# Kernel tuning notes

Hardware: AMD Instinct MI355X
Metric: run time of the kernel (lower is better)

## Reference

```python
import jax, jax.numpy as jnp
import numpy as np

D = 256
H = 8
DK = D // H
FF = 4 * D
EPS = 1e-5


def layer_norm(x, g, b):
    mu = jnp.mean(x, axis=-1, keepdims=True)
    var = jnp.mean(jnp.square(x - mu), axis=-1, keepdims=True)
    return (x - mu) * jax.lax.rsqrt(var + EPS) * g + b


def setup_inputs() -> dict:
    key = jax.random.key(0)
    ks = jax.random.split(key, 12)
    s = 0.02
    return {
        "x": jax.random.normal(ks[0], (4, 2048, D), jnp.float32),
        "Wq": jax.random.normal(ks[1], (D, D), jnp.float32) * s,
        "Wk": jax.random.normal(ks[2], (D, D), jnp.float32) * s,
        "Wv": jax.random.normal(ks[3], (D, D), jnp.float32) * s,
        "Wo": jax.random.normal(ks[4], (D, D), jnp.float32) * s,
        "W1": jax.random.normal(ks[5], (D, FF), jnp.float32) * s,
        "W2": jax.random.normal(ks[6], (D, FF), jnp.float32) * s,
        "Wout": jax.random.normal(ks[7], (FF, D), jnp.float32) * s,
        "g1": jnp.ones((D,), jnp.float32),
        "b1": jnp.zeros((D,), jnp.float32),
        "g2": jnp.ones((D,), jnp.float32),
        "b2": jnp.zeros((D,), jnp.float32),
    }


def reference(x, Wq, Wk, Wv, Wo, W1, W2, Wout, g1, b1, g2, b2):
    B, S, _ = x.shape
    # --- multi-head attention (manual matmul + softmax + matmul) ---
    q = (x @ Wq).reshape(B, S, H, DK).transpose(0, 2, 1, 3)  # [B,H,S,DK]
    k = (x @ Wk).reshape(B, S, H, DK).transpose(0, 2, 1, 3)
    v = (x @ Wv).reshape(B, S, H, DK).transpose(0, 2, 1, 3)
    scores = jnp.einsum("bhqd,bhkd->bhqk", q, k) * (DK ** -0.5)  # [B,H,S,S]
    probs = jax.nn.softmax(scores, axis=-1)
    o = jnp.einsum("bhqk,bhkd->bhqd", probs, v)
    attn = o.transpose(0, 2, 1, 3).reshape(B, S, D) @ Wo
    # --- GLU feedforward with dual LayerNorms ---
    x1 = layer_norm(x + attn, g1, b1)
    xw = jax.nn.silu(x1 @ W1)
    xv = x1 @ W2
    out = (xw * xv) @ Wout
    return layer_norm(x1 + out, g2, b2)
```

## Files before the change

kernel.cpp:

```cpp
#include <hip/hip_runtime.h>

#define D 256
#define H 8
#define DK 32
#define FF 1024
#define SEQ 2048
#define BATCH 4
#define MROWS (BATCH * SEQ)
#define LN_EPS 1e-5f
#define QSCALE (0.1767766952966369f * 1.4426950408889634f)
#define LOG2E 1.4426950408889634f

typedef unsigned short u16;
typedef unsigned int u32;
typedef __attribute__((ext_vector_type(8))) short bf16x8;
typedef __attribute__((ext_vector_type(4))) float f32x4;

#define MFMA16(a, b, c) __builtin_amdgcn_mfma_f32_16x16x32_bf16(a, b, c, 0, 0, 0)

#if __has_builtin(__builtin_amdgcn_exp2f)
#define EXP2(x) __builtin_amdgcn_exp2f(x)
#else
#define EXP2(x) exp2f(x)
#endif
#if __has_builtin(__builtin_amdgcn_rcpf)
#define RCPF(x) __builtin_amdgcn_rcpf(x)
#else
#define RCPF(x) (1.f / (x))
#endif

__device__ __forceinline__ u16 f2bf(float f) {
    union { float f; u32 u; } x; x.f = f;
    u32 r = x.u + 0x7fffu + ((x.u >> 16) & 1u);
    return (u16)(r >> 16);
}
__device__ __forceinline__ u32 pack2(float a, float b) {
    return (u32)f2bf(a) | ((u32)f2bf(b) << 16);
}
__device__ __forceinline__ u32 pktrunc(float a, float b) {
    u32 ua = __builtin_bit_cast(u32, a), ub = __builtin_bit_cast(u32, b);
    return __builtin_amdgcn_perm(ub, ua, 0x07060302u);
}
__device__ __forceinline__ float silu_f(float x) {
    return x * RCPF(1.f + EXP2(-x * LOG2E));
}

__global__ void stage_w(const float* __restrict__ Wq, const float* __restrict__ Wk,
                        const float* __restrict__ Wv, const float* __restrict__ Wo,
                        const float* __restrict__ W1, const float* __restrict__ W2,
                        const float* __restrict__ Wout, u16* __restrict__ dst) {
    __shared__ float T[64][65];
    int bid = blockIdx.x, tid = threadIdx.x;
    const float* src;
    size_t dbase;
    int K, N, tile;
    float sc = 1.f;
    if (bid < 64) {
        int which = bid >> 4;
        tile = bid & 15;
        src = which == 0 ? Wq : which == 1 ? Wk : which == 2 ? Wv : Wo;
        if (which == 0) sc = QSCALE;
        dbase = (size_t)which << 16;
        K = 256; N = 256;
    } else if (bid < 192) {
        int which = (bid - 64) >> 6;
        tile = (bid - 64) & 63;
        src = which ? W2 : W1;
        dbase = 262144 + (size_t)which * 262144;
        K = 256; N = 1024;
    } else {
        tile = bid - 192;
        src = Wout;
        dbase = 786432;
        K = 1024; N = 256;
    }
    int ntn = N >> 6;
    int k0 = (tile / ntn) << 6, n0 = (tile % ntn) << 6;
#pragma unroll
    for (int p = 0; p < 4; p++) {
        int r = p * 16 + (tid >> 4), c = (tid & 15) * 4;
        float4 v = *(const float4*)(src + (size_t)(k0 + r) * N + n0 + c);
        T[c + 0][r] = v.x * sc;
        T[c + 1][r] = v.y * sc;
        T[c + 2][r] = v.z * sc;
        T[c + 3][r] = v.w * sc;
    }
    __syncthreads();
#pragma unroll
    for (int p = 0; p < 4; p++) {
        int n = p * 16 + (tid >> 4), k = (tid & 15) * 4;
        uint2 o;
        o.x = pack2(T[n][k], T[n][k + 1]);
        o.y = pack2(T[n][k + 2], T[n][k + 3]);
        *(uint2*)(dst + dbase + (size_t)(n0 + n) * K + k0 + k) = o;
    }
}

__global__ void gemm_qkv(const float* __restrict__ X, const u16* __restrict__ Bt,
                         u16* __restrict__ Qo, u16* __restrict__ Ko,
                         u16* __restrict__ Vo) {
    int gid = (blockIdx.x * 256 + threadIdx.x) >> 6;
    int lane = threadIdx.x & 63;
    int mt = gid / 12, ng = gid - mt * 12;
    int m0 = mt << 5, n0 = ng << 6;
    int m = lane & 15, quad = lane >> 4;
    const float* xp0 = X + (size_t)(m0 + m) * D + quad * 8;
    const float* xp1 = xp0 + (size_t)16 * D;
    const u16* bp = Bt + (size_t)(n0 + m) * D + quad * 8;
    f32x4 acc[2][4] = {{{0,0,0,0},{0,0,0,0},{0,0,0,0},{0,0,0,0}},
                       {{0,0,0,0},{0,0,0,0},{0,0,0,0},{0,0,0,0}}};
    for (int k0 = 0; k0 < D; k0 += 32) {
        float4 f0 = *(const float4*)(xp0 + k0);
        float4 f1 = *(const float4*)(xp0 + k0 + 4);
        float4 f2 = *(const float4*)(xp1 + k0);
        float4 f3 = *(const float4*)(xp1 + k0 + 4);
        uint4 u0, u1;
        u0.x = pktrunc(f0.x, f0.y); u0.y = pktrunc(f0.z, f0.w);
        u0.z = pktrunc(f1.x, f1.y); u0.w = pktrunc(f1.z, f1.w);
        u1.x = pktrunc(f2.x, f2.y); u1.y = pktrunc(f2.z, f2.w);
        u1.z = pktrunc(f3.x, f3.y); u1.w = pktrunc(f3.z, f3.w);
        bf16x8 a0 = __builtin_bit_cast(bf16x8, u0);
        bf16x8 a1 = __builtin_bit_cast(bf16x8, u1);
#pragma unroll
        for (int t = 0; t < 4; t++) {
            bf16x8 bv = *(const bf16x8*)(bp + (size_t)t * 16 * D + k0);
            acc[0][t] = MFMA16(a0, bv, acc[0][t]);
            acc[1][t] = MFMA16(a1, bv, acc[1][t]);
        }
    }
    int seg = n0 >> 8;
    int nc0 = n0 & 255;
    if (seg < 2) {
        u16* out = seg ? Ko : Qo;
#pragma unroll
        for (int u = 0; u < 2; u++) {
            int row = m0 + u * 16 + (quad << 2);
#pragma unroll
            for (int t = 0; t < 4; t++) {
                int col = nc0 + t * 16 + m;
#pragma unroll
                for (int r = 0; r < 4; r++)
                    out[(size_t)(row + r) * D + col] = f2bf(acc[u][t][r]);
            }
        }
    } else {
#pragma unroll
        for (int u = 0; u < 2; u++) {
            int row = m0 + u * 16 + (quad << 2);
            int b = row >> 11, sl = row & 2047;
#pragma unroll
            for (int t = 0; t < 4; t++) {
                int col = nc0 + t * 16 + m;
                int hh = col >> 5, dk = col & 31;
                size_t base = ((size_t)(b * 8 + hh) * 32 + dk) * SEQ + sl;
                uint2 pk;
                pk.x = pack2(acc[u][t][0], acc[u][t][1]);
                pk.y = pack2(acc[u][t][2], acc[u][t][3]);
                *(uint2*)(Vo + base) = pk;
            }
        }
    }
}

__global__ __launch_bounds__(256, 8)
void attn_mfma(const u16* __restrict__ Q, const u16* __restrict__ Km,
               const u16* __restrict__ Vt, u16* __restrict__ O) {
    __shared__ __align__(16) u16 Kt[2][64][36];
    __shared__ __align__(16) u16 Vl[2][32][68];
    int tid = threadIdx.x;
    int lane = tid & 63;
    int m = lane & 15, quad = lane >> 4;
    int w = tid >> 6;
    int bid = blockIdx.x;
    int qb = bid & 63;
    int bh = bid >> 6;
    int b = bh >> 3, h = bh & 7;
    int q0 = qb * 32 + (w & 1) * 16;
    int hb = w >> 1;
    size_t rowbase = (size_t)b * SEQ;

    bf16x8 qa = *(const bf16x8*)(Q + (rowbase + q0 + m) * D + h * DK + quad * 8);

    const u16* kg = Km + rowbase * D + h * DK;
    const u16* vg = Vt + (size_t)bh * DK * SEQ;

    int krow = tid >> 2, kseg = tid & 3;
    int skv = (krow & 32) | (((krow >> 2) & 3) << 3) | (((krow >> 4) & 1) << 2) | (krow & 3);
    int vrow = tid >> 3, vseg = tid & 7;

    uint4 kreg = *(const uint4*)(kg + (size_t)skv * D + kseg * 8);
    uint4 vreg = *(const uint4*)(vg + (size_t)vrow * SEQ + vseg * 8);
    *(uint4*)(&Kt[0][krow][kseg * 8]) = kreg;
    *(uint4*)(&Vl[0][vrow][vseg * 8]) = vreg;

    f32x4 o0 = {0,0,0,0}, o1 = {0,0,0,0};
    float ls = 0.f;

    for (int i = 0; i < SEQ / 64; i++) {
        int buf = i & 1;
        if (i + 1 < SEQ / 64) {
            int kvn = (i + 1) * 64;
            kreg = *(const uint4*)(kg + (size_t)(kvn + skv) * D + kseg * 8);
            vreg = *(const uint4*)(vg + (size_t)vrow * SEQ + kvn + vseg * 8);
        }
        __syncthreads();
        f32x4 z = {0,0,0,0};
        f32x4 s0, s1;
        {
            bf16x8 kb0 = *(const bf16x8*)(&Kt[buf][(2 * hb) * 16 + m][quad * 8]);
            bf16x8 kb1 = *(const bf16x8*)(&Kt[buf][(2 * hb + 1) * 16 + m][quad * 8]);
            s0 = MFMA16(kb0, qa, z);
            s1 = MFMA16(kb1, qa, z);
        }
        {
            float pa0 = EXP2(s0[0]), pa1 = EXP2(s0[1]);
            float pa2 = EXP2(s0[2]), pa3 = EXP2(s0[3]);
            float pb0 = EXP2(s1[0]), pb1 = EXP2(s1[1]);
            float pb2 = EXP2(s1[2]), pb3 = EXP2(s1[3]);
            ls += ((pa0 + pa1) + (pa2 + pa3)) + ((pb0 + pb1) + (pb2 + pb3));
            uint4 pw;
            pw.x = pktrunc(pa0, pa1);
            pw.y = pktrunc(pa2, pa3);
            pw.z = pktrunc(pb0, pb1);
            pw.w = pktrunc(pb2, pb3);
            bf16x8 pfrag = __builtin_bit_cast(bf16x8, pw);
            bf16x8 vb0 = *(const bf16x8*)(&Vl[buf][m][hb * 32 + quad * 8]);
            bf16x8 vb1 = *(const bf16x8*)(&Vl[buf][16 + m][hb * 32 + quad * 8]);
            o0 = MFMA16(pfrag, vb0, o0);
            o1 = MFMA16(pfrag, vb1, o1);
        }
        if (i + 1 < SEQ / 64) {
            *(uint4*)(&Kt[buf ^ 1][krow][kseg * 8]) = kreg;
            *(uint4*)(&Vl[buf ^ 1][vrow][vseg * 8]) = vreg;
        }
    }
    ls += __shfl_xor(ls, 16);
    ls += __shfl_xor(ls, 32);
    __syncthreads();
    float* comb = (float*)&Kt[0][0][0];
    if (w >= 2) {
        float* c = comb + ((size_t)(w - 2) * 64 + lane) * 9;
#pragma unroll
        for (int r = 0; r < 4; r++) { c[r] = o0[r]; c[4 + r] = o1[r]; }
        c[8] = ls;
    }
    __syncthreads();
    if (w < 2) {
        const float* c = comb + ((size_t)w * 64 + lane) * 9;
#pragma unroll
        for (int r = 0; r < 4; r++) { o0[r] += c[r]; o1[r] += c[4 + r]; }
        ls += c[8];
        u16* ob = O + (rowbase + q0 + quad * 4) * D + h * DK;
#pragma unroll
        for (int r = 0; r < 4; r++) {
            float lr = __shfl(ls, quad * 4 + r);
            float inv = 1.f / lr;
            ob[(size_t)r * D + m] = f2bf(o0[r] * inv);
            ob[(size_t)r * D + 16 + m] = f2bf(o1[r] * inv);
        }
    }
}

__global__ __launch_bounds__(256, 2)
void wo_res_ln(const u16* __restrict__ A, const u16* __restrict__ Bt,
               const float* __restrict__ res, const float* __restrict__ g,
               const float* __restrict__ bb, float* __restrict__ outf) {
    __shared__ float Sy[4][16], Sq[4][16], Mu[16], Rs[16];
    int tid = threadIdx.x;
    int w = tid >> 6, lane = tid & 63;
    int m = lane & 15, quad = lane >> 4;
    int m0 = blockIdx.x << 4, n0 = w << 6;
    const u16* ap = A + (size_t)(m0 + m) * D + quad * 8;
    const u16* bp = Bt + (size_t)(n0 + m) * D + quad * 8;
    f32x4 acc[4] = {{0,0,0,0},{0,0,0,0},{0,0,0,0},{0,0,0,0}};
#pragma unroll
    for (int k0 = 0; k0 < D; k0 += 32) {
        bf16x8 a0 = *(const bf16x8*)(ap + k0);
#pragma unroll
        for (int t = 0; t < 4; t++)
            acc[t] = MFMA16(a0, *(const bf16x8*)(bp + (size_t)t * 16 * D + k0), acc[t]);
    }
#pragma unroll
    for (int r = 0; r < 4; r++) {
        int row = (quad << 2) + r;
        float sy = 0.f, sq = 0.f;
#pragma unroll
        for (int t = 0; t < 4; t++) {
            float y = acc[t][r] + res[(size_t)(m0 + row) * D + n0 + t * 16 + m];
            acc[t][r] = y;
            sy += y;
            sq += y * y;
        }
        sy += __shfl_xor(sy, 1); sq += __shfl_xor(sq, 1);
        sy += __shfl_xor(sy, 2); sq += __shfl_xor(sq, 2);
        sy += __shfl_xor(sy, 4); sq += __shfl_xor(sq, 4);
        sy += __shfl_xor(sy, 8); sq += __shfl_xor(sq, 8);
        if (m == 0) { Sy[w][row] = sy; Sq[w][row] = sq; }
    }
    __syncthreads();
    if (tid < 16) {
        float s = Sy[0][tid] + Sy[1][tid] + Sy[2][tid] + Sy[3][tid];
        float q = Sq[0][tid] + Sq[1][tid] + Sq[2][tid] + Sq[3][tid];
        float mu = s * (1.f / 256.f);
        float var = q * (1.f / 256.f) - mu * mu;
        Mu[tid] = mu;
        Rs[tid] = rsqrtf(var + LN_EPS);
    }
    __syncthreads();
#pragma unroll
    for (int r = 0; r < 4; r++) {
        int row = (quad << 2) + r;
        float mu = Mu[row], rs = Rs[row];
#pragma unroll
        for (int t = 0; t < 4; t++) {
            int col = n0 + t * 16 + m;
            outf[(size_t)(m0 + row) * D + col] = (acc[t][r] - mu) * rs * g[col] + bb[col];
        }
    }
}

__global__ __launch_bounds__(1024, 4)
void ff_fused(const float* __restrict__ x1f, const u16* __restrict__ W1t,
              const u16* __restrict__ W2t, const u16* __restrict__ Woutt,
              const float* __restrict__ g, const float* __restrict__ bb,
              float* __restrict__ outf) {
    __shared__ __align__(16) u16 X1l[32][268];
    __shared__ __align__(16) u16 Gl[32][1044];
    __shared__ float Sy[16][32], Sq[16][32], Mu[32], Rs[32];
    int tid = threadIdx.x;
    int w = tid >> 6, lane = tid & 63;
    int m = lane & 15, quad = lane >> 4;
    int m0 = blockIdx.x << 5;

#pragma unroll
    for (int p = 0; p < 2; p++) {
        int idx = p * 1024 + tid;
        int row = idx >> 6, c = (idx & 63) * 4;
        float4 v = *(const float4*)(x1f + (size_t)(m0 + row) * D + c);
        uint2 o;
        o.x = pack2(v.x, v.y);
        o.y = pack2(v.z, v.w);
        *(uint2*)(&X1l[row][c]) = o;
    }
    __syncthreads();

    {
        int n0 = w << 6;
        const u16* b1 = W1t + (size_t)(n0 + m) * D + quad * 8;
        const u16* b2 = W2t + (size_t)(n0 + m) * D + quad * 8;
        f32x4 a1[2][4] = {{{0,0,0,0},{0,0,0,0},{0,0,0,0},{0,0,0,0}},
                          {{0,0,0,0},{0,0,0,0},{0,0,0,0},{0,0,0,0}}};
        f32x4 a2[2][4] = {{{0,0,0,0},{0,0,0,0},{0,0,0,0},{0,0,0,0}},
                          {{0,0,0,0},{0,0,0,0},{0,0,0,0},{0,0,0,0}}};
#pragma unroll
        for (int k0 = 0; k0 < D; k0 += 32) {
            bf16x8 av0 = *(const bf16x8*)(&X1l[m][k0 + quad * 8]);
            bf16x8 av1 = *(const bf16x8*)(&X1l[16 + m][k0 + quad * 8]);
#pragma unroll
            for (int t = 0; t < 4; t++) {
                bf16x8 w1 = *(const bf16x8*)(b1 + (size_t)t * 16 * D + k0);
                bf16x8 w2 = *(const bf16x8*)(b2 + (size_t)t * 16 * D + k0);
                a1[0][t] = MFMA16(av0, w1, a1[0][t]);
                a1[1][t] = MFMA16(av1, w1, a1[1][t]);
                a2[0][t] = MFMA16(av0, w2, a2[0][t]);
                a2[1][t] = MFMA16(av1, w2, a2[1][t]);
            }
        }
#pragma unroll
        for (int u = 0; u < 2; u++) {
            int row = u * 16 + (quad << 2);
#pragma unroll
            for (int t = 0; t < 4; t++) {
                int col = n0 + t * 16 + m;
#pragma unroll
                for (int r = 0; r < 4; r++)
                    Gl[row + r][col] = f2bf(silu_f(a1[u][t][r]) * a2[u][t][r]);
            }
        }
    }
    __syncthreads();

    int n0p = w << 4;
    const u16* bp = Woutt + (size_t)(n0p + m) * FF + quad * 8;
    f32x4 acc[2] = {{0,0,0,0},{0,0,0,0}};
#pragma unroll 4
    for (int k0 = 0; k0 < FF; k0 += 32) {
        bf16x8 a0 = *(const bf16x8*)(&Gl[m][k0 + quad * 8]);
        bf16x8 a1v = *(const bf16x8*)(&Gl[16 + m][k0 + quad * 8]);
        bf16x8 bv = *(const bf16x8*)(bp + k0);
        acc[0] = MFMA16(a0, bv, acc[0]);
        acc[1] = MFMA16(a1v, bv, acc[1]);
    }
#pragma unroll
    for (int u = 0; u < 2; u++) {
#pragma unroll
        for (int r = 0; r < 4; r++) {
            int row = u * 16 + (quad << 2) + r;
            float y = acc[u][r] + x1f[(size_t)(m0 + row) * D + n0p + m];
            acc[u][r] = y;
            float sy = y, sq = y * y;
            sy += __shfl_xor(sy, 1); sq += __shfl_xor(sq, 1);
            sy += __shfl_xor(sy, 2); sq += __shfl_xor(sq, 2);
            sy += __shfl_xor(sy, 4); sq += __shfl_xor(sq, 4);
            sy += __shfl_xor(sy, 8); sq += __shfl_xor(sq, 8);
            if (m == 0) { Sy[w][row] = sy; Sq[w][row] = sq; }
        }
    }
    __syncthreads();
    if (tid < 32) {
        float s = 0.f, q = 0.f;
#pragma unroll
        for (int ww = 0; ww < 16; ww++) { s += Sy[ww][tid]; q += Sq[ww][tid]; }
        float mu = s * (1.f / 256.f);
        float var = q * (1.f / 256.f) - mu * mu;
        Mu[tid] = mu;
        Rs[tid] = rsqrtf(var + LN_EPS);
    }
    __syncthreads();
#pragma unroll
    for (int u = 0; u < 2; u++) {
#pragma unroll
        for (int r = 0; r < 4; r++) {
            int row = u * 16 + (quad << 2) + r;
            float mu = Mu[row], rs = Rs[row];
            int col = n0p + m;
            outf[(size_t)(m0 + row) * D + col] =
                (acc[u][r] - mu) * rs * g[col] + bb[col];
        }
    }
}

#define WS_WQKVT  ((size_t)0)
#define WS_WOT    ((size_t)196608)
#define WS_W1T    ((size_t)262144)
#define WS_W2T    ((size_t)524288)
#define WS_WOUTT  ((size_t)786432)
#define WS_Q      ((size_t)1048576)
#define WS_K      ((size_t)3145728)
#define WS_VT     ((size_t)5242880)
#define WS_O      ((size_t)7340032)
#define WS_X1F    ((size_t)9437184)

extern "C" void kernel_launch(void* const* d_in, const int* in_sizes, int n_in,
                              void* d_out, int out_size, void* d_ws, size_t ws_size,
                              hipStream_t stream) {
    const float* x    = (const float*)d_in[0];
    const float* Wq   = (const float*)d_in[1];
    const float* Wk   = (const float*)d_in[2];
    const float* Wv   = (const float*)d_in[3];
    const float* Wo   = (const float*)d_in[4];
    const float* W1   = (const float*)d_in[5];
    const float* W2   = (const float*)d_in[6];
    const float* Wout = (const float*)d_in[7];
    const float* g1   = (const float*)d_in[8];
    const float* b1   = (const float*)d_in[9];
    const float* g2   = (const float*)d_in[10];
    const float* b2   = (const float*)d_in[11];

    u16* ws = (u16*)d_ws;
    float* x1f = (float*)(ws + WS_X1F);

    stage_w<<<256, 256, 0, stream>>>(Wq, Wk, Wv, Wo, W1, W2, Wout, ws + WS_WQKVT);

    gemm_qkv<<<768, 256, 0, stream>>>(x, ws + WS_WQKVT,
                                      ws + WS_Q, ws + WS_K, ws + WS_VT);

    attn_mfma<<<2048, 256, 0, stream>>>(ws + WS_Q, ws + WS_K, ws + WS_VT, ws + WS_O);

    wo_res_ln<<<512, 256, 0, stream>>>(ws + WS_O, ws + WS_WOT, x, g1, b1, x1f);

    ff_fused<<<256, 1024, 0, stream>>>(x1f, ws + WS_W1T, ws + WS_W2T, ws + WS_WOUTT,
                                       g2, b2, (float*)d_out);
}
```

Measured before the change: 205.9 us.

## Fuse Wo projection, residual and first LayerNorm into feed-forward kernel

Merges the Wo GEMM, residual add and first LayerNorm into the fused feed-forward kernel, so x1 is produced directly into shared memory as bf16 instead of being written to and re-read from a global fp32 buffer. This removes one kernel launch and the x1 round trip through global memory. In exchange, the second residual now uses the bf16-rounded x1 rather than fp32, a small precision loss. Each 1024-thread block also does the extra Wo work over only 256 blocks.

```diff
diff --git a/kernel.cpp b/kernel.cpp
--- a/kernel.cpp
+++ b/kernel.cpp
@@ -29,6 +29,9 @@
 #define RCPF(x) (1.f / (x))
 #endif
 
+__device__ __forceinline__ float b2f(u16 v) {
+    union { u32 i; float f; } x; x.i = ((u32)v) << 16; return x.f;
+}
 __device__ __forceinline__ u16 f2bf(float f) {
     union { float f; u32 u; } x; x.f = f;
     u32 r = x.u + 0x7fffu + ((x.u >> 16) & 1u);
@@ -261,69 +264,13 @@
     }
 }
 
-__global__ __launch_bounds__(256, 2)
-void wo_res_ln(const u16* __restrict__ A, const u16* __restrict__ Bt,
-               const float* __restrict__ res, const float* __restrict__ g,
-               const float* __restrict__ bb, float* __restrict__ outf) {
-    __shared__ float Sy[4][16], Sq[4][16], Mu[16], Rs[16];
-    int tid = threadIdx.x;
-    int w = tid >> 6, lane = tid & 63;
-    int m = lane & 15, quad = lane >> 4;
-    int m0 = blockIdx.x << 4, n0 = w << 6;
-    const u16* ap = A + (size_t)(m0 + m) * D + quad * 8;
-    const u16* bp = Bt + (size_t)(n0 + m) * D + quad * 8;
-    f32x4 acc[4] = {{0,0,0,0},{0,0,0,0},{0,0,0,0},{0,0,0,0}};
-#pragma unroll
-    for (int k0 = 0; k0 < D; k0 += 32) {
-        bf16x8 a0 = *(const bf16x8*)(ap + k0);
-#pragma unroll
-        for (int t = 0; t < 4; t++)
-            acc[t] = MFMA16(a0, *(const bf16x8*)(bp + (size_t)t * 16 * D + k0), acc[t]);
-    }
-#pragma unroll
-    for (int r = 0; r < 4; r++) {
-        int row = (quad << 2) + r;
-        float sy = 0.f, sq = 0.f;
-#pragma unroll
-        for (int t = 0; t < 4; t++) {
-            float y = acc[t][r] + res[(size_t)(m0 + row) * D + n0 + t * 16 + m];
-            acc[t][r] = y;
-            sy += y;
-            sq += y * y;
-        }
-        sy += __shfl_xor(sy, 1); sq += __shfl_xor(sq, 1);
-        sy += __shfl_xor(sy, 2); sq += __shfl_xor(sq, 2);
-        sy += __shfl_xor(sy, 4); sq += __shfl_xor(sq, 4);
-        sy += __shfl_xor(sy, 8); sq += __shfl_xor(sq, 8);
-        if (m == 0) { Sy[w][row] = sy; Sq[w][row] = sq; }
-    }
-    __syncthreads();
-    if (tid < 16) {
-        float s = Sy[0][tid] + Sy[1][tid] + Sy[2][tid] + Sy[3][tid];
-        float q = Sq[0][tid] + Sq[1][tid] + Sq[2][tid] + Sq[3][tid];
-        float mu = s * (1.f / 256.f);
-        float var = q * (1.f / 256.f) - mu * mu;
-        Mu[tid] = mu;
-        Rs[tid] = rsqrtf(var + LN_EPS);
-    }
-    __syncthreads();
-#pragma unroll
-    for (int r = 0; r < 4; r++) {
-        int row = (quad << 2) + r;
-        float mu = Mu[row], rs = Rs[row];
-#pragma unroll
-        for (int t = 0; t < 4; t++) {
-            int col = n0 + t * 16 + m;
-            outf[(size_t)(m0 + row) * D + col] = (acc[t][r] - mu) * rs * g[col] + bb[col];
-        }
-    }
-}
-
 __global__ __launch_bounds__(1024, 4)
-void ff_fused(const float* __restrict__ x1f, const u16* __restrict__ W1t,
-              const u16* __restrict__ W2t, const u16* __restrict__ Woutt,
-              const float* __restrict__ g, const float* __restrict__ bb,
-              float* __restrict__ outf) {
+void ff_mega(const u16* __restrict__ O, const u16* __restrict__ WoT,
+             const float* __restrict__ x, const float* __restrict__ g1,
+             const float* __restrict__ b1, const u16* __restrict__ W1t,
+             const u16* __restrict__ W2t, const u16* __restrict__ Woutt,
+             const float* __restrict__ g2, const float* __restrict__ b2,
+             float* __restrict__ outf) {
     __shared__ __align__(16) u16 X1l[32][268];
     __shared__ __align__(16) u16 Gl[32][1044];
     __shared__ float Sy[16][32], Sq[16][32], Mu[32], Rs[32];
@@ -332,22 +279,61 @@
     int m = lane & 15, quad = lane >> 4;
     int m0 = blockIdx.x << 5;
 
-#pragma unroll
-    for (int p = 0; p < 2; p++) {
-        int idx = p * 1024 + tid;
-        int row = idx >> 6, c = (idx & 63) * 4;
-        float4 v = *(const float4*)(x1f + (size_t)(m0 + row) * D + c);
-        uint2 o;
-        o.x = pack2(v.x, v.y);
-        o.y = pack2(v.z, v.w);
-        *(uint2*)(&X1l[row][c]) = o;
+    int nA = w << 4;
+    {
+        const u16* ap0 = O + (size_t)(m0 + m) * D + quad * 8;
+        const u16* ap1 = ap0 + (size_t)16 * D;
+        const u16* bp = WoT + (size_t)(nA + m) * D + quad * 8;
+        f32x4 acc[2] = {{0,0,0,0},{0,0,0,0}};
+#pragma unroll
+        for (int k0 = 0; k0 < D; k0 += 32) {
+            bf16x8 bv = *(const bf16x8*)(bp + k0);
+            acc[0] = MFMA16(*(const bf16x8*)(ap0 + k0), bv, acc[0]);
+            acc[1] = MFMA16(*(const bf16x8*)(ap1 + k0), bv, acc[1]);
+        }
+#pragma unroll
+        for (int u = 0; u < 2; u++) {
+#pragma unroll
+            for (int r = 0; r < 4; r++) {
+                int row = u * 16 + (quad << 2) + r;
+                float y = acc[u][r] + x[(size_t)(m0 + row) * D + nA + m];
+                acc[u][r] = y;
+                float sy = y, sq = y * y;
+                sy += __shfl_xor(sy, 1); sq += __shfl_xor(sq, 1);
+                sy += __shfl_xor(sy, 2); sq += __shfl_xor(sq, 2);
+                sy += __shfl_xor(sy, 4); sq += __shfl_xor(sq, 4);
+                sy += __shfl_xor(sy, 8); sq += __shfl_xor(sq, 8);
+                if (m == 0) { Sy[w][row] = sy; Sq[w][row] = sq; }
+            }
+        }
+        __syncthreads();
+        if (tid < 32) {
+            float s = 0.f, q = 0.f;
+#pragma unroll
+            for (int ww = 0; ww < 16; ww++) { s += Sy[ww][tid]; q += Sq[ww][tid]; }
+            float mu = s * (1.f / 256.f);
+            float var = q * (1.f / 256.f) - mu * mu;
+            Mu[tid] = mu;
+            Rs[tid] = rsqrtf(var + LN_EPS);
+        }
+        __syncthreads();
+#pragma unroll
+        for (int u = 0; u < 2; u++) {
+#pragma unroll
+            for (int r = 0; r < 4; r++) {
+                int row = u * 16 + (quad << 2) + r;
+                int col = nA + m;
+                float x1v = (acc[u][r] - Mu[row]) * Rs[row] * g1[col] + b1[col];
+                X1l[row][col] = f2bf(x1v);
+            }
+        }
     }
     __syncthreads();
 
     {
         int n0 = w << 6;
-        const u16* b1 = W1t + (size_t)(n0 + m) * D + quad * 8;
-        const u16* b2 = W2t + (size_t)(n0 + m) * D + quad * 8;
+        const u16* b1p = W1t + (size_t)(n0 + m) * D + quad * 8;
+        const u16* b2p = W2t + (size_t)(n0 + m) * D + quad * 8;
         f32x4 a1[2][4] = {{{0,0,0,0},{0,0,0,0},{0,0,0,0},{0,0,0,0}},
                           {{0,0,0,0},{0,0,0,0},{0,0,0,0},{0,0,0,0}}};
         f32x4 a2[2][4] = {{{0,0,0,0},{0,0,0,0},{0,0,0,0},{0,0,0,0}},
@@ -358,8 +344,8 @@
             bf16x8 av1 = *(const bf16x8*)(&X1l[16 + m][k0 + quad * 8]);
 #pragma unroll
             for (int t = 0; t < 4; t++) {
-                bf16x8 w1 = *(const bf16x8*)(b1 + (size_t)t * 16 * D + k0);
-                bf16x8 w2 = *(const bf16x8*)(b2 + (size_t)t * 16 * D + k0);
+                bf16x8 w1 = *(const bf16x8*)(b1p + (size_t)t * 16 * D + k0);
+                bf16x8 w2 = *(const bf16x8*)(b2p + (size_t)t * 16 * D + k0);
                 a1[0][t] = MFMA16(av0, w1, a1[0][t]);
                 a1[1][t] = MFMA16(av1, w1, a1[1][t]);
                 a2[0][t] = MFMA16(av0, w2, a2[0][t]);
@@ -371,7 +357,7 @@
             int row = u * 16 + (quad << 2);
 #pragma unroll
             for (int t = 0; t < 4; t++) {
-                int col = n0 + t * 16 + m;
+                int col = (w << 6) + t * 16 + m;
 #pragma unroll
                 for (int r = 0; r < 4; r++)
                     Gl[row + r][col] = f2bf(silu_f(a1[u][t][r]) * a2[u][t][r]);
@@ -381,23 +367,24 @@
     __syncthreads();
 
     int n0p = w << 4;
-    const u16* bp = Woutt + (size_t)(n0p + m) * FF + quad * 8;
-    f32x4 acc[2] = {{0,0,0,0},{0,0,0,0}};
+    const u16* bp2 = Woutt + (size_t)(n0p + m) * FF + quad * 8;
+    f32x4 acc2[2] = {{0,0,0,0},{0,0,0,0}};
 #pragma unroll 4
     for (int k0 = 0; k0 < FF; k0 += 32) {
         bf16x8 a0 = *(const bf16x8*)(&Gl[m][k0 + quad * 8]);
         bf16x8 a1v = *(const bf16x8*)(&Gl[16 + m][k0 + quad * 8]);
-        bf16x8 bv = *(const bf16x8*)(bp + k0);
-        acc[0] = MFMA16(a0, bv, acc[0]);
-        acc[1] = MFMA16(a1v, bv, acc[1]);
-    }
+        bf16x8 bv = *(const bf16x8*)(bp2 + k0);
+        acc2[0] = MFMA16(a0, bv, acc2[0]);
+        acc2[1] = MFMA16(a1v, bv, acc2[1]);
+    }
+    __syncthreads();
 #pragma unroll
     for (int u = 0; u < 2; u++) {
 #pragma unroll
         for (int r = 0; r < 4; r++) {
             int row = u * 16 + (quad << 2) + r;
-            float y = acc[u][r] + x1f[(size_t)(m0 + row) * D + n0p + m];
-            acc[u][r] = y;
+            float y = acc2[u][r] + b2f(X1l[row][n0p + m]);
+            acc2[u][r] = y;
             float sy = y, sq = y * y;
             sy += __shfl_xor(sy, 1); sq += __shfl_xor(sq, 1);
             sy += __shfl_xor(sy, 2); sq += __shfl_xor(sq, 2);
@@ -422,10 +409,9 @@
 #pragma unroll
         for (int r = 0; r < 4; r++) {
             int row = u * 16 + (quad << 2) + r;
-            float mu = Mu[row], rs = Rs[row];
             int col = n0p + m;
             outf[(size_t)(m0 + row) * D + col] =
-                (acc[u][r] - mu) * rs * g[col] + bb[col];
+                (acc2[u][r] - Mu[row]) * Rs[row] * g2[col] + b2[col];
         }
     }
 }
@@ -439,7 +425,6 @@
 #define WS_K      ((size_t)3145728)
 #define WS_VT     ((size_t)5242880)
 #define WS_O      ((size_t)7340032)
-#define WS_X1F    ((size_t)9437184)
 
 extern "C" void kernel_launch(void* const* d_in, const int* in_sizes, int n_in,
                               void* d_out, int out_size, void* d_ws, size_t ws_size,
@@ -458,7 +443,6 @@
     const float* b2   = (const float*)d_in[11];
 
     u16* ws = (u16*)d_ws;
-    float* x1f = (float*)(ws + WS_X1F);
 
     stage_w<<<256, 256, 0, stream>>>(Wq, Wk, Wv, Wo, W1, W2, Wout, ws + WS_WQKVT);
 
@@ -467,8 +451,7 @@
 
     attn_mfma<<<2048, 256, 0, stream>>>(ws + WS_Q, ws + WS_K, ws + WS_VT, ws + WS_O);
 
-    wo_res_ln<<<512, 256, 0, stream>>>(ws + WS_O, ws + WS_WOT, x, g1, b1, x1f);
-
-    ff_fused<<<256, 1024, 0, stream>>>(x1f, ws + WS_W1T, ws + WS_W2T, ws + WS_WOUTT,
-                                       g2, b2, (float*)d_out);
-}
+    ff_mega<<<256, 1024, 0, stream>>>(ws + WS_O, ws + WS_WOT, x, g1, b1,
+                                      ws + WS_W1T, ws + WS_W2T, ws + WS_WOUTT,
+                                      g2, b2, (float*)d_out);
+}
```

After: 214.8 us. +4.3%, slower.

## Split fused feedforward into weight-stationary GLU kernel and Wout+LN kernel

Applied to the files above, without the earlier changes.

The fused FF kernel, which reloaded W1/W2 from global memory for every 32-row block, is split in two. The new GLU kernel keeps a 64-column W1/W2 slab in LDS and sweeps 512 rows per block, writing the gated activations to a bf16 workspace buffer. A second kernel reads those activations into LDS and performs the Wout GEMM with the residual add and LayerNorm. wo_res_ln now also writes a bf16 copy of x1 so the GLU kernel skips the float-to-bf16 conversion. In exchange there is an extra kernel launch and an 8192x1024 bf16 intermediate that must round-trip through global memory, reusing the Q workspace region.

```diff
diff --git a/kernel.cpp b/kernel.cpp
--- a/kernel.cpp
+++ b/kernel.cpp
@@ -264,7 +264,8 @@
 __global__ __launch_bounds__(256, 2)
 void wo_res_ln(const u16* __restrict__ A, const u16* __restrict__ Bt,
                const float* __restrict__ res, const float* __restrict__ g,
-               const float* __restrict__ bb, float* __restrict__ outf) {
+               const float* __restrict__ bb, float* __restrict__ outf,
+               u16* __restrict__ outb) {
     __shared__ float Sy[4][16], Sq[4][16], Mu[16], Rs[16];
     int tid = threadIdx.x;
     int w = tid >> 6, lane = tid & 63;
@@ -314,72 +315,89 @@
 #pragma unroll
         for (int t = 0; t < 4; t++) {
             int col = n0 + t * 16 + m;
-            outf[(size_t)(m0 + row) * D + col] = (acc[t][r] - mu) * rs * g[col] + bb[col];
+            float yv = (acc[t][r] - mu) * rs * g[col] + bb[col];
+            outf[(size_t)(m0 + row) * D + col] = yv;
+            outb[(size_t)(m0 + row) * D + col] = f2bf(yv);
+        }
+    }
+}
+
+__global__ __launch_bounds__(512, 2)
+void glu_ws(const u16* __restrict__ x1b, const u16* __restrict__ W1t,
+            const u16* __restrict__ W2t, u16* __restrict__ G) {
+    __shared__ __align__(16) u16 WL[2][64][260];
+    int tid = threadIdx.x;
+    int w = tid >> 6, lane = tid & 63;
+    int m = lane & 15, quad = lane >> 4;
+    int cg = blockIdx.x & 15, rg = blockIdx.x >> 4;
+    int n0 = cg << 6;
+#pragma unroll
+    for (int i = 0; i < 4; i++) {
+        int idx = i * 512 + tid;
+        int row = idx >> 5, seg = idx & 31;
+        *(uint4*)(&WL[0][row][seg * 8]) =
+            *(const uint4*)(W1t + (size_t)(n0 + row) * D + seg * 8);
+        *(uint4*)(&WL[1][row][seg * 8]) =
+            *(const uint4*)(W2t + (size_t)(n0 + row) * D + seg * 8);
+    }
+    __syncthreads();
+    int mr = rg * 512 + w * 64;
+    f32x4 a1[4][4], a2[4][4];
+#pragma unroll
+    for (int u = 0; u < 4; u++)
+#pragma unroll
+        for (int t = 0; t < 4; t++) {
+            a1[u][t] = (f32x4){0.f, 0.f, 0.f, 0.f};
+            a2[u][t] = (f32x4){0.f, 0.f, 0.f, 0.f};
+        }
+#pragma unroll
+    for (int k0 = 0; k0 < D; k0 += 32) {
+        bf16x8 av[4];
+#pragma unroll
+        for (int u = 0; u < 4; u++)
+            av[u] = *(const bf16x8*)(x1b + (size_t)(mr + u * 16 + m) * D + k0 + quad * 8);
+#pragma unroll
+        for (int t = 0; t < 4; t++) {
+            bf16x8 w1 = *(const bf16x8*)(&WL[0][t * 16 + m][k0 + quad * 8]);
+            bf16x8 w2 = *(const bf16x8*)(&WL[1][t * 16 + m][k0 + quad * 8]);
+#pragma unroll
+            for (int u = 0; u < 4; u++) {
+                a1[u][t] = MFMA16(av[u], w1, a1[u][t]);
+                a2[u][t] = MFMA16(av[u], w2, a2[u][t]);
+            }
+        }
+    }
+#pragma unroll
+    for (int u = 0; u < 4; u++) {
+        int row = mr + u * 16 + (quad << 2);
+#pragma unroll
+        for (int t = 0; t < 4; t++) {
+            int col = n0 + t * 16 + m;
+#pragma unroll
+            for (int r = 0; r < 4; r++)
+                G[(size_t)(row + r) * FF + col] = f2bf(silu_f(a1[u][t][r]) * a2[u][t][r]);
         }
     }
 }
 
 __global__ __launch_bounds__(1024, 4)
-void ff_fused(const float* __restrict__ x1f, const u16* __restrict__ W1t,
-              const u16* __restrict__ W2t, const u16* __restrict__ Woutt,
-              const float* __restrict__ g, const float* __restrict__ bb,
-              float* __restrict__ outf) {
-    __shared__ __align__(16) u16 X1l[32][268];
+void wout_ln(const u16* __restrict__ G, const u16* __restrict__ Woutt,
+             const float* __restrict__ x1f, const float* __restrict__ g,
+             const float* __restrict__ bb, float* __restrict__ outf) {
     __shared__ __align__(16) u16 Gl[32][1044];
     __shared__ float Sy[16][32], Sq[16][32], Mu[32], Rs[32];
     int tid = threadIdx.x;
     int w = tid >> 6, lane = tid & 63;
     int m = lane & 15, quad = lane >> 4;
     int m0 = blockIdx.x << 5;
-
-#pragma unroll
-    for (int p = 0; p < 2; p++) {
-        int idx = p * 1024 + tid;
-        int row = idx >> 6, c = (idx & 63) * 4;
-        float4 v = *(const float4*)(x1f + (size_t)(m0 + row) * D + c);
-        uint2 o;
-        o.x = pack2(v.x, v.y);
-        o.y = pack2(v.z, v.w);
-        *(uint2*)(&X1l[row][c]) = o;
-    }
-    __syncthreads();
-
-    {
-        int n0 = w << 6;
-        const u16* b1 = W1t + (size_t)(n0 + m) * D + quad * 8;
-        const u16* b2 = W2t + (size_t)(n0 + m) * D + quad * 8;
-        f32x4 a1[2][4] = {{{0,0,0,0},{0,0,0,0},{0,0,0,0},{0,0,0,0}},
-                          {{0,0,0,0},{0,0,0,0},{0,0,0,0},{0,0,0,0}}};
-        f32x4 a2[2][4] = {{{0,0,0,0},{0,0,0,0},{0,0,0,0},{0,0,0,0}},
-                          {{0,0,0,0},{0,0,0,0},{0,0,0,0},{0,0,0,0}}};
-#pragma unroll
-        for (int k0 = 0; k0 < D; k0 += 32) {
-            bf16x8 av0 = *(const bf16x8*)(&X1l[m][k0 + quad * 8]);
-            bf16x8 av1 = *(const bf16x8*)(&X1l[16 + m][k0 + quad * 8]);
-#pragma unroll
-            for (int t = 0; t < 4; t++) {
-                bf16x8 w1 = *(const bf16x8*)(b1 + (size_t)t * 16 * D + k0);
-                bf16x8 w2 = *(const bf16x8*)(b2 + (size_t)t * 16 * D + k0);
-                a1[0][t] = MFMA16(av0, w1, a1[0][t]);
-                a1[1][t] = MFMA16(av1, w1, a1[1][t]);
-                a2[0][t] = MFMA16(av0, w2, a2[0][t]);
-                a2[1][t] = MFMA16(av1, w2, a2[1][t]);
-            }
-        }
-#pragma unroll
-        for (int u = 0; u < 2; u++) {
-            int row = u * 16 + (quad << 2);
-#pragma unroll
-            for (int t = 0; t < 4; t++) {
-                int col = n0 + t * 16 + m;
-#pragma unroll
-                for (int r = 0; r < 4; r++)
-                    Gl[row + r][col] = f2bf(silu_f(a1[u][t][r]) * a2[u][t][r]);
-            }
-        }
-    }
-    __syncthreads();
-
+#pragma unroll
+    for (int i = 0; i < 4; i++) {
+        int idx = i * 1024 + tid;
+        int row = idx >> 7, seg = idx & 127;
+        *(uint4*)(&Gl[row][seg * 8]) =
+            *(const uint4*)(G + (size_t)(m0 + row) * FF + seg * 8);
+    }
+    __syncthreads();
     int n0p = w << 4;
     const u16* bp = Woutt + (size_t)(n0p + m) * FF + quad * 8;
     f32x4 acc[2] = {{0,0,0,0},{0,0,0,0}};
@@ -422,10 +440,9 @@
 #pragma unroll
         for (int r = 0; r < 4; r++) {
             int row = u * 16 + (quad << 2) + r;
-            float mu = Mu[row], rs = Rs[row];
             int col = n0p + m;
             outf[(size_t)(m0 + row) * D + col] =
-                (acc[u][r] - mu) * rs * g[col] + bb[col];
+                (acc[u][r] - Mu[row]) * Rs[row] * g[col] + bb[col];
         }
     }
 }
@@ -439,7 +456,9 @@
 #define WS_K      ((size_t)3145728)
 #define WS_VT     ((size_t)5242880)
 #define WS_O      ((size_t)7340032)
+#define WS_GATED  ((size_t)1048576)
 #define WS_X1F    ((size_t)9437184)
+#define WS_X1B    ((size_t)13631488)
 
 extern "C" void kernel_launch(void* const* d_in, const int* in_sizes, int n_in,
                               void* d_out, int out_size, void* d_ws, size_t ws_size,
@@ -467,8 +486,12 @@
 
     attn_mfma<<<2048, 256, 0, stream>>>(ws + WS_Q, ws + WS_K, ws + WS_VT, ws + WS_O);
 
-    wo_res_ln<<<512, 256, 0, stream>>>(ws + WS_O, ws + WS_WOT, x, g1, b1, x1f);
-
-    ff_fused<<<256, 1024, 0, stream>>>(x1f, ws + WS_W1T, ws + WS_W2T, ws + WS_WOUTT,
-                                       g2, b2, (float*)d_out);
-}
+    wo_res_ln<<<512, 256, 0, stream>>>(ws + WS_O, ws + WS_WOT, x, g1, b1,
+                                       x1f, ws + WS_X1B);
+
+    glu_ws<<<256, 512, 0, stream>>>(ws + WS_X1B, ws + WS_W1T, ws + WS_W2T,
+                                    ws + WS_GATED);
+
+    wout_ln<<<256, 1024, 0, stream>>>(ws + WS_GATED, ws + WS_WOUTT, x1f,
+                                      g2, b2, (float*)d_out);
+}
```

After: 195.0 us. -5.3%, faster.
